# Performance work log

Hardware: AMD Instinct MI355X
Metric: run time of the kernel (lower is better)

## Reference

```python
import jax, jax.numpy as jnp
import numpy as np

SIZE = 224
SCALE = (0.1, 1.0)
RATIO = (0.8, 1.25)
N_TRIES = 10


def _get_params(key, H, W):
    """Batched RandomResizedCrop params. H, W: int32 [B]. Returns int32 (i, j, h, w)."""
    B = H.shape[0]
    Hf = H.astype(jnp.float32)
    Wf = W.astype(jnp.float32)
    area = Hf * Wf
    log_lo = np.log(RATIO[0]).astype(np.float32)
    log_hi = np.log(RATIO[1]).astype(np.float32)
    final_h = jnp.full((B,), -1.0, dtype=jnp.float32)
    final_w = jnp.full((B,), -1.0, dtype=jnp.float32)
    final_i = jnp.full((B,), -1.0, dtype=jnp.float32)
    final_j = jnp.full((B,), -1.0, dtype=jnp.float32)
    success = jnp.zeros((B,), dtype=bool)
    for t in range(N_TRIES):  # fixed small trip count, matches torch loop
        k1, k2, k3, k4 = jax.random.split(jax.random.fold_in(key, t), 4)
        target_area = area * jax.random.uniform(k1, (B,), minval=SCALE[0], maxval=SCALE[1])
        aspect = jnp.exp(jax.random.uniform(k2, (B,), minval=log_lo, maxval=log_hi))
        crop_w = jnp.round(jnp.sqrt(target_area * aspect))
        crop_h = jnp.round(jnp.sqrt(target_area / aspect))
        valid = (crop_w > 0) & (crop_w <= Wf) & (crop_h > 0) & (crop_h <= Hf) & (~success)
        max_i = jnp.clip(Hf - crop_h + 1.0, 1.0, None)
        max_j = jnp.clip(Wf - crop_w + 1.0, 1.0, None)
        rand_i = jnp.floor(jax.random.uniform(k3, (B,)) * max_i)
        rand_j = jnp.floor(jax.random.uniform(k4, (B,)) * max_j)
        final_h = jnp.where(valid, crop_h, final_h)
        final_w = jnp.where(valid, crop_w, final_w)
        final_i = jnp.where(valid, rand_i, final_i)
        final_j = jnp.where(valid, rand_j, final_j)
        success = success | valid
    # center-crop fallback for failed samples
    failed = ~success
    in_ratio = Wf / Hf
    fb_w = jnp.where(in_ratio > RATIO[1], jnp.round(Hf * RATIO[1]), Wf)
    fb_h = jnp.where(in_ratio < RATIO[0], jnp.round(Wf / RATIO[0]), Hf)
    fb_i = jnp.floor((Hf - fb_h) / 2.0)
    fb_j = jnp.floor((Wf - fb_w) / 2.0)
    final_h = jnp.where(failed, fb_h, final_h)
    final_w = jnp.where(failed, fb_w, final_w)
    final_i = jnp.where(failed, fb_i, final_i)
    final_j = jnp.where(failed, fb_j, final_j)
    return (final_i.astype(jnp.int32), final_j.astype(jnp.int32),
            final_h.astype(jnp.int32), final_w.astype(jnp.int32))


def _bilinear_crop_resize(img, i, j, h, w):
    """Crop img[C,Hm,Wm] at (i,j,h,w) then bilinear-resize to (SIZE,SIZE).
    Matches torch F.interpolate(bilinear, align_corners=False) coordinate mapping."""
    C, Hm, Wm = img.shape
    hf = h.astype(jnp.float32)
    wf = w.astype(jnp.float32)
    # source coords within the crop, clamped as torch does
    ys = jnp.clip((jnp.arange(SIZE, dtype=jnp.float32) + 0.5) * hf / SIZE - 0.5, 0.0, hf - 1.0)
    xs = jnp.clip((jnp.arange(SIZE, dtype=jnp.float32) + 0.5) * wf / SIZE - 0.5, 0.0, wf - 1.0)
    y0f = jnp.floor(ys); x0f = jnp.floor(xs)
    wy = ys - y0f; wx = xs - x0f
    y0 = jnp.clip(y0f.astype(jnp.int32) + i, 0, Hm - 1)
    y1 = jnp.clip(y0 + 1, 0, jnp.clip(i + h - 1, 0, Hm - 1))
    x0 = jnp.clip(x0f.astype(jnp.int32) + j, 0, Wm - 1)
    x1 = jnp.clip(x0 + 1, 0, jnp.clip(j + w - 1, 0, Wm - 1))
    g00 = img[:, y0[:, None], x0[None, :]]  # [C,SIZE,SIZE]
    g01 = img[:, y0[:, None], x1[None, :]]
    g10 = img[:, y1[:, None], x0[None, :]]
    g11 = img[:, y1[:, None], x1[None, :]]
    top = (1.0 - wx)[None, None, :] * g00 + wx[None, None, :] * g01
    bot = (1.0 - wx)[None, None, :] * g10 + wx[None, None, :] * g11
    return (1.0 - wy)[None, :, None] * top + wy[None, :, None] * bot


def setup_inputs() -> dict:
    B, C, Hm, Wm_meta = 64, 3, 512, 513
    key = jax.random.key(0)
    k1, k2, k3 = jax.random.split(key, 3)
    x = jax.random.normal(k1, (B, C, Hm, Wm_meta), dtype=jnp.float32)
    H_orig = jax.random.randint(k2, (B,), 256, Hm + 1).astype(jnp.float32)
    W_orig = jax.random.randint(k3, (B,), 256, (Wm_meta - 1) + 1).astype(jnp.float32)
    # metadata column: per-sample original dims
    x = x.at[:, 0, 0, -1].set(H_orig)
    x = x.at[:, 1, 0, -1].set(W_orig)
    return {"x": x}


def reference(x):
    B, C, Hm, Wm_meta = x.shape
    Wm = Wm_meta - 1
    # decode original dims from metadata (before flip, as in torch code)
    H = x[:, 0, 0, -1].astype(jnp.int32)
    W = x[:, 1, 0, -1].astype(jnp.int32)
    key = jax.random.key(42)
    kflip, kparams = jax.random.split(key)
    flip_mask = jax.random.uniform(kflip, (B,)) > 0.5
    # hflip the full tensor (including meta column), faithful to original
    x = jnp.where(flip_mask[:, None, None, None], x[:, :, :, ::-1], x)
    i, j, h, w = _get_params(kparams, H, W)
    x_no_meta = x[:, :, :, :Wm]
    return jax.vmap(_bilinear_crop_resize)(x_no_meta, i, j, h, w)
```

## Files before the change

kernel.cpp:

```cpp
#include <hip/hip_runtime.h>
#include <stdint.h>

#define B_DIM 64
#define C_DIM 3
#define HM 512
#define WM_META 513
#define WM 512
#define OSIZE 224
#define N_TRIES 10
#define OX_UNITS (OSIZE / 4)
#define UNITS_PER_B (C_DIM * OSIZE * OX_UNITS)
#define BLOCKS_PER_B (UNITS_PER_B / 256)

__device__ __forceinline__ uint32_t rotl32(uint32_t v, int d) {
    return (v << d) | (v >> (32 - d));
}

__device__ __forceinline__ void threefry2x32(uint32_t k0, uint32_t k1,
                                             uint32_t x0, uint32_t x1,
                                             uint32_t& o0, uint32_t& o1) {
    const uint32_t ks0 = k0, ks1 = k1, ks2 = k0 ^ k1 ^ 0x1BD11BDAu;
    x0 += ks0; x1 += ks1;
    x0 += x1; x1 = rotl32(x1, 13); x1 ^= x0;
    x0 += x1; x1 = rotl32(x1, 15); x1 ^= x0;
    x0 += x1; x1 = rotl32(x1, 26); x1 ^= x0;
    x0 += x1; x1 = rotl32(x1,  6); x1 ^= x0;
    x0 += ks1; x1 += ks2 + 1u;
    x0 += x1; x1 = rotl32(x1, 17); x1 ^= x0;
    x0 += x1; x1 = rotl32(x1, 29); x1 ^= x0;
    x0 += x1; x1 = rotl32(x1, 16); x1 ^= x0;
    x0 += x1; x1 = rotl32(x1, 24); x1 ^= x0;
    x0 += ks2; x1 += ks0 + 2u;
    x0 += x1; x1 = rotl32(x1, 13); x1 ^= x0;
    x0 += x1; x1 = rotl32(x1, 15); x1 ^= x0;
    x0 += x1; x1 = rotl32(x1, 26); x1 ^= x0;
    x0 += x1; x1 = rotl32(x1,  6); x1 ^= x0;
    x0 += ks0; x1 += ks1 + 3u;
    x0 += x1; x1 = rotl32(x1, 17); x1 ^= x0;
    x0 += x1; x1 = rotl32(x1, 29); x1 ^= x0;
    x0 += x1; x1 = rotl32(x1, 16); x1 ^= x0;
    x0 += x1; x1 = rotl32(x1, 24); x1 ^= x0;
    x0 += ks1; x1 += ks2 + 4u;
    x0 += x1; x1 = rotl32(x1, 13); x1 ^= x0;
    x0 += x1; x1 = rotl32(x1, 15); x1 ^= x0;
    x0 += x1; x1 = rotl32(x1, 26); x1 ^= x0;
    x0 += x1; x1 = rotl32(x1,  6); x1 ^= x0;
    x0 += ks2; x1 += ks0 + 5u;
    o0 = x0; o1 = x1;
}

__device__ __forceinline__ uint32_t jax_bits_elem(uint32_t k0, uint32_t k1, int b) {
    uint32_t w0, w1;
    threefry2x32(k0, k1, 0u, (uint32_t)b, w0, w1);
    return w0 ^ w1;
}

__device__ __forceinline__ float bits_to_uniform(uint32_t bits, float lo, float hi) {
#pragma clang fp contract(off)
    uint32_t fb = (bits >> 9) | 0x3f800000u;
    float u = __uint_as_float(fb) - 1.0f;
    float d = hi - lo;
    float v = u * d + lo;
    return fmaxf(lo, v);
}

__global__ void __launch_bounds__(256)
fused_kernel(const float* __restrict__ x, float* __restrict__ out) {
#pragma clang fp contract(off)
    __shared__ float u_lds[41];

    const int tid = threadIdx.x;
    const int b = blockIdx.x / BLOCKS_PER_B;

    if (tid < 41) {
        if (tid < 40) {
            int t = tid >> 2;
            int q = tid & 3;
            uint32_t kp0, kp1;
            threefry2x32(0u, 42u, 0u, 1u, kp0, kp1);
            uint32_t f0, f1;
            threefry2x32(kp0, kp1, 0u, (uint32_t)t, f0, f1);
            uint32_t kq0, kq1;
            threefry2x32(f0, f1, 0u, (uint32_t)q, kq0, kq1);
            uint32_t bits = jax_bits_elem(kq0, kq1, b);
            const float log_lo = -0.22314355131420976f;
            const float log_hi =  0.22314355131420976f;
            float lo = (q == 0) ? 0.1f : (q == 1) ? log_lo : 0.0f;
            float hi = (q == 0) ? 1.0f : (q == 1) ? log_hi : 1.0f;
            u_lds[tid] = bits_to_uniform(bits, lo, hi);
        } else {
            uint32_t kf0, kf1;
            threefry2x32(0u, 42u, 0u, 0u, kf0, kf1);
            uint32_t bits = jax_bits_elem(kf0, kf1, b);
            u_lds[40] = bits_to_uniform(bits, 0.0f, 1.0f);
        }
    }
    __syncthreads();

    size_t base = (size_t)b * C_DIM * HM * WM_META;
    float Hf = x[base + (WM_META - 1)];
    float Wf = x[base + (size_t)HM * WM_META + (WM_META - 1)];
    float area = Hf * Wf;

    int flip = (u_lds[40] > 0.5f) ? 1 : 0;

    float fi = -1.0f, fj = -1.0f, fh = -1.0f, fw = -1.0f;
    bool success = false;
    for (int t = 0; t < N_TRIES; ++t) {
        float u1 = u_lds[t * 4 + 0];
        float u2 = u_lds[t * 4 + 1];
        float u3 = u_lds[t * 4 + 2];
        float u4 = u_lds[t * 4 + 3];

        float ta = area * u1;
        float aspect = expf(u2);
        float cw = rintf(sqrtf(ta * aspect));
        float ch = rintf(sqrtf(ta / aspect));

        bool valid = (cw > 0.0f) && (cw <= Wf) && (ch > 0.0f) && (ch <= Hf) && (!success);

        float max_i = fmaxf(Hf - ch + 1.0f, 1.0f);
        float max_j = fmaxf(Wf - cw + 1.0f, 1.0f);
        float ri = floorf(u3 * max_i);
        float rj = floorf(u4 * max_j);

        if (valid) { fh = ch; fw = cw; fi = ri; fj = rj; success = true; }
    }
    if (!success) {
        float in_ratio = Wf / Hf;
        float fbw = (in_ratio > 1.25f) ? rintf(Hf * 1.25f) : Wf;
        float fbh = (in_ratio < 0.8f)  ? rintf(Wf / 0.8f)  : Hf;
        fi = floorf((Hf - fbh) / 2.0f);
        fj = floorf((Wf - fbw) / 2.0f);
        fh = fbh; fw = fbw;
    }

    int pi = (int)fi, pj = (int)fj, ph = (int)fh, pw = (int)fw;

    int idx = blockIdx.x * 256 + tid;
    int oxu = idx % OX_UNITS;
    int tmp = idx / OX_UNITS;
    int oy = tmp % OSIZE;
    tmp /= OSIZE;
    int c = tmp % C_DIM;

    float hf = (float)ph, wf = (float)pw;

    float ys = ((float)oy + 0.5f) * hf;
    ys = ys / 224.0f;
    ys = ys - 0.5f;
    ys = fminf(fmaxf(ys, 0.0f), hf - 1.0f);
    float y0f = floorf(ys);
    float wy = ys - y0f;
    int y0 = (int)y0f + pi;
    y0 = min(max(y0, 0), HM - 1);
    int yhi = min(max(pi + ph - 1, 0), HM - 1);
    int y1 = min(max(y0 + 1, 0), yhi);

    int xhi = min(max(pj + pw - 1, 0), WM - 1);

    const float* img  = x + ((size_t)(b * C_DIM + c)) * HM * WM_META;
    const float* row0 = img + (size_t)y0 * WM_META;
    const float* row1 = img + (size_t)y1 * WM_META;

    float res[4];
#pragma unroll
    for (int k = 0; k < 4; ++k) {
        int ox = oxu * 4 + k;
        float xs = ((float)ox + 0.5f) * wf;
        xs = xs / 224.0f;
        xs = xs - 0.5f;
        xs = fminf(fmaxf(xs, 0.0f), wf - 1.0f);
        float x0f = floorf(xs);
        float wx = xs - x0f;
        int x0 = (int)x0f + pj;
        x0 = min(max(x0, 0), WM - 1);
        int x1 = min(max(x0 + 1, 0), xhi);

        int mx0 = flip ? (WM - x0) : x0;
        int mx1 = flip ? (WM - x1) : x1;

        float g00 = row0[mx0];
        float g01 = row0[mx1];
        float g10 = row1[mx0];
        float g11 = row1[mx1];

        float top = (1.0f - wx) * g00 + wx * g01;
        float bot = (1.0f - wx) * g10 + wx * g11;
        res[k] = (1.0f - wy) * top + wy * bot;
    }

    float4 v = make_float4(res[0], res[1], res[2], res[3]);
    *reinterpret_cast<float4*>(out + (size_t)idx * 4) = v;
}

extern "C" void kernel_launch(void* const* d_in, const int* in_sizes, int n_in,
                              void* d_out, int out_size, void* d_ws, size_t ws_size,
                              hipStream_t stream) {
    const float* x = (const float*)d_in[0];
    float* out = (float*)d_out;

    const int blocks = B_DIM * BLOCKS_PER_B;
    fused_kernel<<<blocks, 256, 0, stream>>>(x, out);
}
```

Before: 274.8 us.

## Split into per-sample params kernel writing lookup tables and lean resize kernel

Crop-parameter generation (threefry RNG, the 10-try loop) and the per-row and per-column bilinear coordinates now run once per sample in a small kernel that writes y0/y1/wy and mirrored x0/x1/wx tables to workspace. Before, every block of the resize repeated that work. The resize kernel reads the tables with vector loads, gathers the pixels and writes with nontemporal stores. In exchange it adds a second launch with a serial dependency and a workspace round trip, and it falls back to the fused kernel when no workspace is provided.

After: 269.6 us. No clear change (-1.9%).

```diff
diff --git a/kernel.cpp b/kernel.cpp
--- a/kernel.cpp
+++ b/kernel.cpp
@@ -11,6 +11,10 @@
 #define OX_UNITS (OSIZE / 4)
 #define UNITS_PER_B (C_DIM * OSIZE * OX_UNITS)
 #define BLOCKS_PER_B (UNITS_PER_B / 256)
+#define TBL_STRIDE (B_DIM * OSIZE)
+#define WS_NEEDED (6u * TBL_STRIDE * 4u)
+
+typedef float f32x4_t __attribute__((ext_vector_type(4)));
 
 __device__ __forceinline__ uint32_t rotl32(uint32_t v, int d) {
     return (v << d) | (v >> (32 - d));
@@ -65,12 +69,12 @@
 }
 
 __global__ void __launch_bounds__(256)
-fused_kernel(const float* __restrict__ x, float* __restrict__ out) {
+params_kernel(const float* __restrict__ x, float* __restrict__ ws) {
 #pragma clang fp contract(off)
     __shared__ float u_lds[41];
 
     const int tid = threadIdx.x;
-    const int b = blockIdx.x / BLOCKS_PER_B;
+    const int b = blockIdx.x;
 
     if (tid < 41) {
         if (tid < 40) {
@@ -137,6 +141,182 @@
 
     int pi = (int)fi, pj = (int)fj, ph = (int)fh, pw = (int)fw;
 
+    if (tid < OSIZE) {
+        float hf = (float)ph;
+        int oy = tid;
+        float ys = ((float)oy + 0.5f) * hf;
+        ys = ys / 224.0f;
+        ys = ys - 0.5f;
+        ys = fminf(fmaxf(ys, 0.0f), hf - 1.0f);
+        float y0f = floorf(ys);
+        float wy = ys - y0f;
+        int y0 = (int)y0f + pi;
+        y0 = min(max(y0, 0), HM - 1);
+        int yhi = min(max(pi + ph - 1, 0), HM - 1);
+        int y1 = min(max(y0 + 1, 0), yhi);
+
+        int*   ty0 = (int*)ws;
+        int*   ty1 = (int*)(ws + TBL_STRIDE);
+        float* twy = ws + 2 * TBL_STRIDE;
+        int off = b * OSIZE + tid;
+        ty0[off] = y0;
+        ty1[off] = y1;
+        twy[off] = wy;
+
+        float wf = (float)pw;
+        int ox = tid;
+        float xs = ((float)ox + 0.5f) * wf;
+        xs = xs / 224.0f;
+        xs = xs - 0.5f;
+        xs = fminf(fmaxf(xs, 0.0f), wf - 1.0f);
+        float x0f = floorf(xs);
+        float wx = xs - x0f;
+        int x0 = (int)x0f + pj;
+        x0 = min(max(x0, 0), WM - 1);
+        int xhi = min(max(pj + pw - 1, 0), WM - 1);
+        int x1 = min(max(x0 + 1, 0), xhi);
+
+        int mx0 = flip ? (WM - x0) : x0;
+        int mx1 = flip ? (WM - x1) : x1;
+
+        int*   tmx0 = (int*)(ws + 3 * TBL_STRIDE);
+        int*   tmx1 = (int*)(ws + 4 * TBL_STRIDE);
+        float* twx  = ws + 5 * TBL_STRIDE;
+        tmx0[off] = mx0;
+        tmx1[off] = mx1;
+        twx[off]  = wx;
+    }
+}
+
+__global__ void __launch_bounds__(256)
+resize_kernel(const float* __restrict__ x, const float* __restrict__ ws,
+              float* __restrict__ out) {
+#pragma clang fp contract(off)
+    const int tid = threadIdx.x;
+    const int idx = blockIdx.x * 256 + tid;
+    const int b = blockIdx.x / BLOCKS_PER_B;
+
+    int oxu = idx % OX_UNITS;
+    int tmp = idx / OX_UNITS;
+    int oy = tmp % OSIZE;
+    int c = (tmp / OSIZE) % C_DIM;
+
+    const int*   ty0  = (const int*)ws;
+    const int*   ty1  = (const int*)(ws + TBL_STRIDE);
+    const float* twy  = ws + 2 * TBL_STRIDE;
+    const int*   tmx0 = (const int*)(ws + 3 * TBL_STRIDE);
+    const int*   tmx1 = (const int*)(ws + 4 * TBL_STRIDE);
+    const float* twx  = ws + 5 * TBL_STRIDE;
+
+    const int yoff = b * OSIZE + oy;
+    const int y0 = ty0[yoff];
+    const int y1 = ty1[yoff];
+    const float wy = twy[yoff];
+
+    const int xoff = b * OSIZE + oxu * 4;
+    const int4   m0  = *reinterpret_cast<const int4*>(tmx0 + xoff);
+    const int4   m1  = *reinterpret_cast<const int4*>(tmx1 + xoff);
+    const float4 wxv = *reinterpret_cast<const float4*>(twx + xoff);
+
+    const float* img  = x + ((size_t)(b * C_DIM + c)) * HM * WM_META;
+    const float* row0 = img + (size_t)y0 * WM_META;
+    const float* row1 = img + (size_t)y1 * WM_META;
+
+    const int   mx0a[4] = {m0.x, m0.y, m0.z, m0.w};
+    const int   mx1a[4] = {m1.x, m1.y, m1.z, m1.w};
+    const float wxa[4]  = {wxv.x, wxv.y, wxv.z, wxv.w};
+
+    float res[4];
+#pragma unroll
+    for (int k = 0; k < 4; ++k) {
+        float g00 = row0[mx0a[k]];
+        float g01 = row0[mx1a[k]];
+        float g10 = row1[mx0a[k]];
+        float g11 = row1[mx1a[k]];
+
+        float top = (1.0f - wxa[k]) * g00 + wxa[k] * g01;
+        float bot = (1.0f - wxa[k]) * g10 + wxa[k] * g11;
+        res[k] = (1.0f - wy) * top + wy * bot;
+    }
+
+    f32x4_t v;
+    v.x = res[0]; v.y = res[1]; v.z = res[2]; v.w = res[3];
+    __builtin_nontemporal_store(v, reinterpret_cast<f32x4_t*>(out + (size_t)idx * 4));
+}
+
+__global__ void __launch_bounds__(256)
+fused_kernel(const float* __restrict__ x, float* __restrict__ out) {
+#pragma clang fp contract(off)
+    __shared__ float u_lds[41];
+
+    const int tid = threadIdx.x;
+    const int b = blockIdx.x / BLOCKS_PER_B;
+
+    if (tid < 41) {
+        if (tid < 40) {
+            int t = tid >> 2;
+            int q = tid & 3;
+            uint32_t kp0, kp1;
+            threefry2x32(0u, 42u, 0u, 1u, kp0, kp1);
+            uint32_t f0, f1;
+            threefry2x32(kp0, kp1, 0u, (uint32_t)t, f0, f1);
+            uint32_t kq0, kq1;
+            threefry2x32(f0, f1, 0u, (uint32_t)q, kq0, kq1);
+            uint32_t bits = jax_bits_elem(kq0, kq1, b);
+            const float log_lo = -0.22314355131420976f;
+            const float log_hi =  0.22314355131420976f;
+            float lo = (q == 0) ? 0.1f : (q == 1) ? log_lo : 0.0f;
+            float hi = (q == 0) ? 1.0f : (q == 1) ? log_hi : 1.0f;
+            u_lds[tid] = bits_to_uniform(bits, lo, hi);
+        } else {
+            uint32_t kf0, kf1;
+            threefry2x32(0u, 42u, 0u, 0u, kf0, kf1);
+            uint32_t bits = jax_bits_elem(kf0, kf1, b);
+            u_lds[40] = bits_to_uniform(bits, 0.0f, 1.0f);
+        }
+    }
+    __syncthreads();
+
+    size_t base = (size_t)b * C_DIM * HM * WM_META;
+    float Hf = x[base + (WM_META - 1)];
+    float Wf = x[base + (size_t)HM * WM_META + (WM_META - 1)];
+    float area = Hf * Wf;
+
+    int flip = (u_lds[40] > 0.5f) ? 1 : 0;
+
+    float fi = -1.0f, fj = -1.0f, fh = -1.0f, fw = -1.0f;
+    bool success = false;
+    for (int t = 0; t < N_TRIES; ++t) {
+        float u1 = u_lds[t * 4 + 0];
+        float u2 = u_lds[t * 4 + 1];
+        float u3 = u_lds[t * 4 + 2];
+        float u4 = u_lds[t * 4 + 3];
+
+        float ta = area * u1;
+        float aspect = expf(u2);
+        float cw = rintf(sqrtf(ta * aspect));
+        float ch = rintf(sqrtf(ta / aspect));
+
+        bool valid = (cw > 0.0f) && (cw <= Wf) && (ch > 0.0f) && (ch <= Hf) && (!success);
+
+        float max_i = fmaxf(Hf - ch + 1.0f, 1.0f);
+        float max_j = fmaxf(Wf - cw + 1.0f, 1.0f);
+        float ri = floorf(u3 * max_i);
+        float rj = floorf(u4 * max_j);
+
+        if (valid) { fh = ch; fw = cw; fi = ri; fj = rj; success = true; }
+    }
+    if (!success) {
+        float in_ratio = Wf / Hf;
+        float fbw = (in_ratio > 1.25f) ? rintf(Hf * 1.25f) : Wf;
+        float fbh = (in_ratio < 0.8f)  ? rintf(Wf / 0.8f)  : Hf;
+        fi = floorf((Hf - fbh) / 2.0f);
+        fj = floorf((Wf - fbw) / 2.0f);
+        fh = fbh; fw = fbw;
+    }
+
+    int pi = (int)fi, pj = (int)fj, ph = (int)fh, pw = (int)fw;
+
     int idx = blockIdx.x * 256 + tid;
     int oxu = idx % OX_UNITS;
     int tmp = idx / OX_UNITS;
@@ -201,5 +381,12 @@
     float* out = (float*)d_out;
 
     const int blocks = B_DIM * BLOCKS_PER_B;
-    fused_kernel<<<blocks, 256, 0, stream>>>(x, out);
-}
+
+    if (d_ws != nullptr && ws_size >= (size_t)WS_NEEDED) {
+        float* ws = (float*)d_ws;
+        params_kernel<<<B_DIM, 256, 0, stream>>>(x, ws);
+        resize_kernel<<<blocks, 256, 0, stream>>>(x, ws, out);
+    } else {
+        fused_kernel<<<blocks, 256, 0, stream>>>(x, out);
+    }
+}
```
